# Kernel tuning notes

Measured on AMD Instinct MI355X. Metric: run time of the kernel, lower is better.

Reference implementation:

```python
import jax, jax.numpy as jnp
import numpy as np

B = 64        # graphs per batch
H = 8         # heads
EH = 16       # each_head = ceil(128/8)
HD = 128      # h_dimension
N_DA = 100000
N_Q = 20000
E_DA = 1000000
E_Q = 200000
EPS = 1e-5    # BatchNorm1d eps
SLOPE = 2.0   # leaky_relu_GAT_rate


def setup_inputs() -> dict:
    key = jax.random.key(0)
    ks = jax.random.split(key, 24)
    r = lambda i, shape, s=1.0: jax.random.normal(ks[i], shape, dtype=jnp.float32) * s
    return {
        'h_da_last': r(0, (N_DA, HD)),
        'h_q_last': r(1, (N_Q, HD)),
        'h_da_0': r(2, (N_DA, HD)),
        'h_q_0': r(3, (N_Q, HD)),
        'W_L': r(4, (HD, HD), 0.05), 'b_L': jnp.zeros((HD,), jnp.float32),
        'gateq_W': r(5, (HD, 1), 0.05), 'gateq_b': jnp.zeros((1,), jnp.float32),
        'gate1_W': r(6, (HD, 1), 0.05), 'gate1_b': jnp.zeros((1,), jnp.float32),
        'gate2_W': r(7, (HD, 1), 0.05), 'gate2_b': jnp.zeros((1,), jnp.float32),
        'Q_comb': r(8, (1, HD), 0.1),
        'Qf_W1': r(9, (HD, 2 * HD), 0.05), 'Qf_b1': jnp.zeros((2 * HD,), jnp.float32),
        'Qf_W2': r(10, (2 * HD, 2 * H * EH), 0.05), 'Qf_b2': jnp.zeros((2 * H * EH,), jnp.float32),
        'end_W1': r(11, (H * EH, 2 * HD), 0.05), 'end_b1': jnp.zeros((2 * HD,), jnp.float32),
        'end_W2': r(12, (2 * HD, HD), 0.05), 'end_b2': jnp.zeros((HD,), jnp.float32),
        'src_da': jax.random.randint(ks[13], (E_DA,), 0, N_DA),
        'dst_da': jax.random.randint(ks[14], (E_DA,), 0, N_DA),
        'src_q': jax.random.randint(ks[15], (E_Q,), 0, N_Q),
        'dst_q': jax.random.randint(ks[16], (E_Q,), 0, N_Q),
        'gid_da': jnp.sort(jax.random.randint(ks[17], (N_DA,), 0, B)),
        'gid_q': jnp.sort(jax.random.randint(ks[18], (N_Q,), 0, B)),
        'PEid': jax.random.randint(ks[19], (100000,), 0, E_DA),
        'DEid': jax.random.randint(ks[20], (100000,), 0, E_DA),
        'len_Mn': 5,
    }


def _bn(y):
    # BatchNorm1d(affine=False), training mode: biased batch stats
    mu = jnp.mean(y, axis=0)
    var = jnp.mean((y - mu) ** 2, axis=0)
    return (y - mu) / jnp.sqrt(var + EPS)


def _fnn(x, W1, b1, W2, b2):
    y = jax.nn.elu(_bn(x @ W1 + b1))
    return jax.nn.elu(_bn(y @ W2 + b2))


def _gap(W, b, feat, gid):
    # GlobalAttentionPooling: softmax(gate) over nodes per graph, weighted sum
    g = (feat @ W + b)[:, 0]                               # [N]
    m = jax.ops.segment_max(g, gid, num_segments=B)
    e = jnp.exp(g - m[gid])
    s = jax.ops.segment_sum(e, gid, num_segments=B)
    w = e / s[gid]
    return jax.ops.segment_sum(w[:, None] * feat, gid, num_segments=B)  # [B, HD]


def _edge_softmax(e, dst, n):
    # softmax over incoming edges per destination node, per head. e: [E, H, 1]
    m = jax.ops.segment_max(e, dst, num_segments=n)
    ex = jnp.exp(e - m[dst])
    s = jax.ops.segment_sum(ex, dst, num_segments=n)
    return ex / s[dst]


def forward(h_da_last, h_q_last, h_da_0, h_q_0, W_L, b_L, gateq_W, gateq_b,
            gate1_W, gate1_b, gate2_W, gate2_b, Q_comb, Qf_W1, Qf_b1, Qf_W2, Qf_b2,
            end_W1, end_b1, end_W2, end_b2,
            src_da, dst_da, src_q, dst_q, gid_da, gid_q, PEid, DEid, len_Mn):
    tmp_q = h_q_last  # MM is None branch

    # graph-level query representation -> per-graph attention queries Q [B, H, 2*EH]
    glq = _gap(gateq_W, gateq_b, h_q_last, gid_q)
    Q = _fnn(glq, Qf_W1, Qf_b1, Qf_W2, Qf_b2).reshape(B, H, 2 * EH)

    def att_comb(M1, M2, gid):
        # ATTpolling_for_3Dtensor with shared Q_comb
        k1 = _gap(gate1_W, gate1_b, M1, gid)
        k2 = _gap(gate2_W, gate2_b, M2, gid)
        s = jnp.stack([(Q_comb * k1).sum(-1), (Q_comb * k2).sum(-1)], axis=-1)  # [B, 2]
        a = jax.nn.softmax(s, axis=-1)[gid]                                     # [N, 2]
        return M1 * a[:, 0:1] + M2 * a[:, 1:2]

    def branch(h_last, tmp, h0, M2, src, dst, gid, n):
        Qn = Q[gid]                                  # [n, H, 2*EH]
        Ql, Qr = Qn[..., :EH], Qn[..., EH:]
        feat = (tmp @ W_L + b_L).reshape(n, H, EH)
        el = (feat * Ql).sum(-1, keepdims=True)      # [n, H, 1]
        er = (feat * Qr).sum(-1, keepdims=True)
        fh = att_comb(h0, M2, gid)
        ft = (fh @ W_L + b_L).reshape(n, H, EH)
        e = jax.nn.leaky_relu(el[src] + er[dst], negative_slope=SLOPE)  # [E, H, 1]
        a = _edge_softmax(e, dst, n)
        agg = jax.ops.segment_sum(ft[src] * a, dst, num_segments=n)     # [n, H, EH]
        out = _fnn(agg.reshape(n, H * EH), end_W1, end_b1, end_W2, end_b2)
        return h_last + out, a                       # residual=True

    h_q_next, _ = branch(h_q_last, tmp_q, h_q_0, h_q_last + (h_q_last - tmp_q),
                         src_q, dst_q, gid_q, N_Q)
    h_da_next, a_da = branch(h_da_last, h_da_last, h_da_0, h_da_last,
                             src_da, dst_da, gid_da, N_DA)

    PE = a_da[PEid].sum(axis=0)                      # [H, 1]
    DE = a_da[DEid].sum(axis=0)
    loss = -1.0 * jnp.mean((PE - DE) / len_Mn, axis=0).reshape(1, 1)
    return h_da_next, h_q_next, loss


def reference(h_da_last, h_q_last, h_da_0, h_q_0, W_L, b_L, gateq_W, gateq_b,
              gate1_W, gate1_b, gate2_W, gate2_b, Q_comb, Qf_W1, Qf_b1, Qf_W2, Qf_b2,
              end_W1, end_b1, end_W2, end_b2,
              src_da, dst_da, src_q, dst_q, gid_da, gid_q, PEid, DEid, len_Mn):
    return forward(h_da_last, h_q_last, h_da_0, h_q_0, W_L, b_L, gateq_W, gateq_b,
                   gate1_W, gate1_b, gate2_W, gate2_b, Q_comb, Qf_W1, Qf_b1, Qf_W2, Qf_b2,
                   end_W1, end_b1, end_W2, end_b2,
                   src_da, dst_da, src_q, dst_q, gid_da, gid_q, PEid, DEid, len_Mn)
```

## Files before the change

kernel.cpp:

```cpp
#include <hip/hip_runtime.h>
#include <math.h>

static constexpr int CB   = 64;
static constexpr int CH   = 8;
static constexpr int CEH  = 16;
static constexpr int CHD  = 128;
static constexpr int CNDA = 100000;
static constexpr int CNQ  = 20000;
static constexpr int CEDA = 1000000;
static constexpr int CEQ  = 200000;
static constexpr float CEPS = 1e-5f;
static constexpr float CSLOPE = 2.0f;

typedef unsigned short ushortt;
typedef __attribute__((ext_vector_type(8))) short bf16x8;
typedef __attribute__((ext_vector_type(4))) float f32x4;

__device__ __forceinline__ float ldf(const float* p) { return *p; }
__device__ __forceinline__ float ldf(const ushortt* p) {
  return __uint_as_float(((unsigned)*p) << 16);
}
__device__ __forceinline__ void stf(float* p, float v) { *p = v; }
__device__ __forceinline__ void stf(ushortt* p, float v) {
  unsigned u = __float_as_uint(v);
  u += 0x7fff + ((u >> 16) & 1);
  *p = (ushortt)(u >> 16);
}
__device__ __forceinline__ short f2bf(float v) {
  unsigned u = __float_as_uint(v);
  u += 0x7fff + ((u >> 16) & 1);
  return (short)(u >> 16);
}
__device__ __forceinline__ float bf2f(short b) {
  return __uint_as_float(((unsigned)(ushortt)b) << 16);
}

__global__ void k_zero(float* __restrict__ p, long n) {
  long i = (long)blockIdx.x * blockDim.x + threadIdx.x;
  long stride = (long)gridDim.x * blockDim.x;
  for (; i < n; i += stride) p[i] = 0.f;
}
static inline void zero_launch(void* p, long n, hipStream_t s) {
  long b = (n + 255) / 256;
  int blocks = (int)(b > 4096 ? 4096 : (b < 1 ? 1 : b));
  hipLaunchKernelGGL(k_zero, dim3(blocks), dim3(256), 0, s, (float*)p, n);
}

__global__ void k_binit(int* start, int n) {
  int i = threadIdx.x;
  if (i <= CB) start[i] = n;
}
__global__ void k_bmark(const int* __restrict__ gid, int n, int* __restrict__ start) {
  int i = blockIdx.x * blockDim.x + threadIdx.x;
  if (i >= n) return;
  int g = gid[i];
  if (i == 0 || gid[i - 1] != g) atomicMin(&start[g], i);
}
__global__ void k_bfix(int* start) {
  if (threadIdx.x == 0) {
    for (int g = CB - 1; g >= 0; --g)
      if (start[g] > start[g + 1]) start[g] = start[g + 1];
  }
}

__global__ void k_gate_dot(const float* __restrict__ feat, const float* __restrict__ gw,
                           const float* __restrict__ gb, float* __restrict__ g, int n) {
  int wave = (blockIdx.x * blockDim.x + threadIdx.x) >> 6;
  int lane = threadIdx.x & 63;
  if (wave >= n) return;
  const float* row = feat + (size_t)wave * CHD;
  float v = row[lane] * gw[lane] + row[lane + 64] * gw[lane + 64];
  for (int off = 32; off > 0; off >>= 1) v += __shfl_down(v, off, 64);
  if (lane == 0) g[wave] = v + gb[0];
}

__global__ void k_gate_dot2(const float* __restrict__ feat,
                            const float* __restrict__ w1, const float* __restrict__ b1,
                            const float* __restrict__ w2, const float* __restrict__ b2,
                            float* __restrict__ g1, float* __restrict__ g2, int n) {
  int wave = (blockIdx.x * blockDim.x + threadIdx.x) >> 6;
  int lane = threadIdx.x & 63;
  if (wave >= n) return;
  const float* row = feat + (size_t)wave * CHD;
  float r0 = row[lane], r1 = row[lane + 64];
  float v1 = r0 * w1[lane] + r1 * w1[lane + 64];
  float v2 = r0 * w2[lane] + r1 * w2[lane + 64];
  for (int off = 32; off > 0; off >>= 1) {
    v1 += __shfl_down(v1, off, 64);
    v2 += __shfl_down(v2, off, 64);
  }
  if (lane == 0) {
    g1[wave] = v1 + b1[0];
    g2[wave] = v2 + b2[0];
  }
}

__global__ void k_gmax5(const float* __restrict__ gq, const int* __restrict__ startq,
                        const int* __restrict__ startda, float* __restrict__ m) {
  int job = blockIdx.x >> 6, grp = blockIdx.x & 63;
  const float* g;
  const int* start;
  if (job == 0)      { g = gq;                              start = startq; }
  else if (job == 1) { g = gq + 2 * (size_t)CNQ;            start = startq; }
  else if (job == 2) { g = gq + (size_t)CNQ;                start = startq; }
  else if (job == 3) { g = gq + 3 * (size_t)CNQ;            start = startda; }
  else               { g = gq + 3 * (size_t)CNQ + CNDA;     start = startda; }
  int s0 = start[grp], s1 = start[grp + 1];
  int t = threadIdx.x;
  __shared__ float red[256];
  float v = -1e30f;
  for (int i = s0 + t; i < s1; i += 256) v = fmaxf(v, g[i]);
  red[t] = v;
  __syncthreads();
  for (int o = 128; o > 0; o >>= 1) {
    if (t < o) red[t] = fmaxf(red[t], red[t + o]);
    __syncthreads();
  }
  if (t == 0) m[job * 64 + grp] = red[0];
}

template <int NG>
__global__ __launch_bounds__(128) void k_gap_partial(
    const float* __restrict__ g0, const float* __restrict__ g1,
    const float* __restrict__ feat, const int* __restrict__ start,
    const float* __restrict__ m,
    float* __restrict__ acc0, float* __restrict__ acc1,
    float* __restrict__ sums) {
  int grp = blockIdx.x;
  int s0 = start[grp], s1 = start[grp + 1];
  int len = s1 - s0;
  if (len <= 0) return;
  int NC = gridDim.y;
  int per = (len + NC - 1) / NC;
  int r0 = s0 + blockIdx.y * per;
  int r1 = min(s1, r0 + per);
  if (r0 >= r1) return;
  int t = threadIdx.x;
  float m0 = m[grp];
  float m1 = (NG == 2) ? m[64 + grp] : 0.f;
  float a0 = 0.f, a1 = 0.f, sum0 = 0.f, sum1 = 0.f;
  for (int i = r0; i < r1; ++i) {
    float f = feat[(size_t)i * CHD + t];
    float e0 = expf(g0[i] - m0);
    sum0 += e0;
    a0 += e0 * f;
    if (NG == 2) {
      float e1 = expf(g1[i] - m1);
      sum1 += e1;
      a1 += e1 * f;
    }
  }
  atomicAdd(&acc0[grp * CHD + t], a0);
  if (NG == 2) atomicAdd(&acc1[grp * CHD + t], a1);
  if (t == 0) {
    atomicAdd(&sums[grp], sum0);
    if (NG == 2) atomicAdd(&sums[64 + grp], sum1);
  }
}

__global__ void k_gap_norm5(float* __restrict__ glq, const float* __restrict__ sbuf) {
  int job = blockIdx.x >> 6, grp = blockIdx.x & 63;
  int t = threadIdx.x;
  int smap = (job == 1) ? 2 : ((job == 2) ? 1 : job);
  float sv = sbuf[smap * 64 + grp];
  float* acc = glq + (size_t)job * CB * CHD + grp * CHD;
  float v = acc[t];
  acc[t] = (sv > 0.f) ? v / sv : 0.f;
}

__global__ void k_mm_small(const float* __restrict__ X, const float* __restrict__ W,
                           const float* __restrict__ bias, float* __restrict__ Y,
                           int m, int k, int p) {
  int idx = blockIdx.x * blockDim.x + threadIdx.x;
  if (idx >= m * p) return;
  int r = idx / p, c = idx % p;
  const float* xr = X + (size_t)r * k;
  const float* wc = W + c;
  float acc = bias[c];
  int kk = 0;
  for (; kk + 8 <= k; kk += 8) {
    float xv[8], wv[8];
#pragma unroll
    for (int j = 0; j < 8; ++j) {
      xv[j] = xr[kk + j];
      wv[j] = wc[(size_t)(kk + j) * p];
    }
#pragma unroll
    for (int j = 0; j < 8; ++j) acc += xv[j] * wv[j];
  }
  for (; kk < k; ++kk) acc += xr[kk] * wc[(size_t)kk * p];
  Y[idx] = acc;
}

__global__ void k_bn_elu_small(float* __restrict__ Y, int m, int p) {
  int c = blockIdx.x * blockDim.x + threadIdx.x;
  if (c >= p) return;
  float s = 0.f, s2 = 0.f;
  int i = 0;
  for (; i + 8 <= m; i += 8) {
    float v[8];
#pragma unroll
    for (int j = 0; j < 8; ++j) v[j] = Y[(size_t)(i + j) * p + c];
#pragma unroll
    for (int j = 0; j < 8; ++j) { s += v[j]; s2 += v[j] * v[j]; }
  }
  for (; i < m; ++i) {
    float v = Y[(size_t)i * p + c];
    s += v; s2 += v * v;
  }
  float mu = s / m;
  float var = s2 / m - mu * mu;
  float inv = rsqrtf(var + CEPS);
  i = 0;
  for (; i + 8 <= m; i += 8) {
    float v[8];
#pragma unroll
    for (int j = 0; j < 8; ++j) v[j] = Y[(size_t)(i + j) * p + c];
#pragma unroll
    for (int j = 0; j < 8; ++j) {
      float x = (v[j] - mu) * inv;
      Y[(size_t)(i + j) * p + c] = x > 0.f ? x : expm1f(x);
    }
  }
  for (; i < m; ++i) {
    float x = (Y[(size_t)i * p + c] - mu) * inv;
    Y[(size_t)i * p + c] = x > 0.f ? x : expm1f(x);
  }
}

__global__ void k_attcomb(const float* __restrict__ k1, const float* __restrict__ k2,
                          const float* __restrict__ Qc, float* __restrict__ a) {
  int grp = blockIdx.x;
  int t = threadIdx.x;
  float v1 = Qc[t] * k1[grp * CHD + t] + Qc[t + 64] * k1[grp * CHD + t + 64];
  float v2 = Qc[t] * k2[grp * CHD + t] + Qc[t + 64] * k2[grp * CHD + t + 64];
  for (int off = 32; off > 0; off >>= 1) {
    v1 += __shfl_down(v1, off, 64);
    v2 += __shfl_down(v2, off, 64);
  }
  if (t == 0) {
    float mx = fmaxf(v1, v2);
    float e1 = expf(v1 - mx), e2 = expf(v2 - mx);
    float s = e1 + e2;
    a[grp * 2] = e1 / s;
    a[grp * 2 + 1] = e2 / s;
  }
}

__global__ void k_wq(const float* __restrict__ W_L, const float* __restrict__ b_L,
                     const float* __restrict__ Qm, float* __restrict__ WQ,
                     float* __restrict__ bQ) {
  int g = blockIdx.x;
  int t = threadIdx.x;
  for (int j = 0; j < 8; ++j) {
    int idx = t + j * 256;
    int d = idx >> 4, c = idx & 15;
    int h = c & 7, off = (c >= 8) ? CEH : 0;
    const float* w = W_L + d * CHD + h * CEH;
    const float* q = Qm + g * 256 + h * 32 + off;
    float acc = 0.f;
#pragma unroll
    for (int e = 0; e < CEH; ++e) acc += w[e] * q[e];
    WQ[g * 2048 + idx] = acc;
  }
  if (t < 16) {
    int c = t, h = c & 7, off = (c >= 8) ? CEH : 0;
    const float* b = b_L + h * CEH;
    const float* q = Qm + g * 256 + h * 32 + off;
    float acc = 0.f;
#pragma unroll
    for (int e = 0; e < CEH; ++e) acc += b[e] * q[e];
    bQ[g * 16 + c] = acc;
  }
}

__global__ void k_eler(const float* __restrict__ tmp, const float* __restrict__ WQ,
                       const float* __restrict__ bQ, const int* __restrict__ gid,
                       float* __restrict__ elr, int n) {
  int idx = blockIdx.x * blockDim.x + threadIdx.x;
  if (idx >= n * 16) return;
  int i = idx >> 4, c = idx & 15;
  int g = gid[i];
  const float* wq = WQ + g * 2048 + c;
  const float* row = tmp + (size_t)i * CHD;
  float acc = bQ[g * 16 + c];
#pragma unroll 4
  for (int d = 0; d < CHD; ++d) acc += row[d] * wq[d * 16];
  elr[idx] = acc;
}

__global__ void k_tcast(const float* __restrict__ W, ushortt* __restrict__ WT,
                        int K, int P) {
  int i = blockIdx.x * blockDim.x + threadIdx.x;
  if (i >= K * P) return;
  int p = i / K, k = i % K;
  stf(&WT[i], W[(size_t)k * P + p]);
}

template <int P>
__global__ void k_bn_prep(const float* __restrict__ stats, float* __restrict__ pr, int n) {
  int c = threadIdx.x;
  if (c >= P) return;
  float invn = 1.f / (float)n;
  float mu = stats[c] * invn;
  float var = stats[P + c] * invn - mu * mu;
  pr[c] = mu;
  pr[P + c] = rsqrtf(var + CEPS);
}

template <int TP>
__global__ void k_stats_reduce(const float* __restrict__ pstat, float* __restrict__ stats,
                               int nb) {
  int c = blockIdx.x * blockDim.x + threadIdx.x;
  if (c >= TP) return;
  int NC = gridDim.y;
  int per = (nb + NC - 1) / NC;
  int r0 = blockIdx.y * per;
  int r1 = min(nb, r0 + per);
  if (r0 >= r1) return;
  float s0 = 0.f, s1 = 0.f, s2 = 0.f, s3 = 0.f;
  int r = r0;
  for (; r + 4 <= r1; r += 4) {
    s0 += pstat[(size_t)(r + 0) * TP + c];
    s1 += pstat[(size_t)(r + 1) * TP + c];
    s2 += pstat[(size_t)(r + 2) * TP + c];
    s3 += pstat[(size_t)(r + 3) * TP + c];
  }
  for (; r < r1; ++r) s0 += pstat[(size_t)r * TP + c];
  atomicAdd(&stats[c], (s0 + s1) + (s2 + s3));
}

template <int K, int P, int XM, bool STATS, typename OT>
__global__ __launch_bounds__(256, 2) void k_gemm_mfma(
    const void* __restrict__ X0v, const void* __restrict__ X1v,
    const float* __restrict__ acomb, const int* __restrict__ gid,
    const float* __restrict__ bnmu, const float* __restrict__ bninv,
    const ushortt* __restrict__ BT, const float* __restrict__ bias,
    OT* __restrict__ Y, float* __restrict__ pstat, int n) {
  constexpr int NT = P / 16;
  const int wave = threadIdx.x >> 6, lane = threadIdx.x & 63;
  const int quad = lane >> 4, l16 = lane & 15;
  const int r0w = blockIdx.x * 64 + wave * 16;
  const int rA = r0w + l16;
  const bool rowok = rA < n;
  f32x4 acc[NT];
#pragma unroll
  for (int t = 0; t < NT; ++t) acc[t] = f32x4{0.f, 0.f, 0.f, 0.f};
  float a0 = 0.f, a1 = 0.f;
  if (XM == 1 && rowok) {
    int g = gid[rA];
    a0 = acomb[2 * g];
    a1 = acomb[2 * g + 1];
  }
  for (int k0 = 0; k0 < K; k0 += 32) {
    const int kk = k0 + quad * 8;
    bf16x8 af = {};
    if (rowok) {
      if constexpr (XM == 2) {
        af = *(const bf16x8*)((const ushortt*)X0v + (size_t)rA * K + kk);
      } else if constexpr (XM == 3) {
        bf16x8 raw = *(const bf16x8*)((const ushortt*)X0v + (size_t)rA * K + kk);
#pragma unroll
        for (int j = 0; j < 8; ++j) {
          float v = bf2f(raw[j]);
          v = (v - bnmu[kk + j]) * bninv[kk + j];
          v = v > 0.f ? v : (__expf(v) - 1.f);
          af[j] = f2bf(v);
        }
      } else {
        const float* px = (const float*)X0v + (size_t)rA * K + kk;
        float v[8];
        if constexpr (XM == 1) {
          const float* py = (const float*)X1v + (size_t)rA * K + kk;
#pragma unroll
          for (int j = 0; j < 8; ++j) v[j] = a0 * px[j] + a1 * py[j];
        } else {
#pragma unroll
          for (int j = 0; j < 8; ++j) v[j] = px[j];
        }
#pragma unroll
        for (int j = 0; j < 8; ++j) af[j] = f2bf(v[j]);
      }
    }
    bf16x8 bfr[NT];
#pragma unroll
    for (int t = 0; t < NT; ++t)
      bfr[t] = *(const bf16x8*)(BT + (size_t)(t * 16 + l16) * K + kk);
#pragma unroll
    for (int t = 0; t < NT; ++t)
      acc[t] = __builtin_amdgcn_mfma_f32_16x16x32_bf16(af, bfr[t], acc[t], 0, 0, 0);
  }
  float* pw = STATS ? (pstat + ((size_t)blockIdx.x * 4 + wave) * (2 * P)) : nullptr;
#pragma unroll
  for (int t = 0; t < NT; ++t) {
    const int c = t * 16 + l16;
    float b = bias[c];
    float s = 0.f, s2 = 0.f;
#pragma unroll
    for (int r = 0; r < 4; ++r) {
      int gr = r0w + quad * 4 + r;
      if (gr < n) {
        float val = acc[t][r] + b;
        stf(Y + (size_t)gr * P + c, val);
        if constexpr (STATS) {
          float vq = (sizeof(OT) == 2) ? bf2f(f2bf(val)) : val;
          s += vq;
          s2 += vq * vq;
        }
      }
    }
    if constexpr (STATS) {
      s += __shfl_xor(s, 16, 64);
      s += __shfl_xor(s, 32, 64);
      s2 += __shfl_xor(s2, 16, 64);
      s2 += __shfl_xor(s2, 32, 64);
      if (quad == 0) {
        pw[c] = s;
        pw[P + c] = s2;
      }
    }
  }
}

__global__ void k_count(const int* __restrict__ dst, int* __restrict__ counts, int E) {
  int e = blockIdx.x * blockDim.x + threadIdx.x;
  if (e < E) atomicAdd(&counts[dst[e]], 1);
}
__global__ void k_scan_reduce(const int* __restrict__ counts, int* __restrict__ bsum, int n) {
  __shared__ int red[256];
  int t = threadIdx.x;
  int base = blockIdx.x * 1024;
  int s = 0;
  for (int j = 0; j < 4; ++j) {
    int i = base + t * 4 + j;
    if (i < n) s += counts[i];
  }
  red[t] = s;
  __syncthreads();
  for (int o = 128; o > 0; o >>= 1) {
    if (t < o) red[t] += red[t + o];
    __syncthreads();
  }
  if (t == 0) bsum[blockIdx.x] = red[0];
}
__global__ void k_scan_top(int* __restrict__ bsum, int nb) {
  __shared__ int sh[128];
  int t = threadIdx.x;
  int v = (t < nb) ? bsum[t] : 0;
  sh[t] = v;
  __syncthreads();
  for (int o = 1; o < 128; o <<= 1) {
    int x = (t >= o) ? sh[t - o] : 0;
    __syncthreads();
    sh[t] += x;
    __syncthreads();
  }
  if (t < nb) bsum[t] = sh[t] - v;
}
__global__ void k_scan_final(const int* __restrict__ counts, const int* __restrict__ bsum,
                             int* __restrict__ rowptr, int n, int E) {
  __shared__ int sh[256];
  int t = threadIdx.x;
  int base = blockIdx.x * 1024;
  int v[4];
  int s = 0;
  for (int j = 0; j < 4; ++j) {
    int i = base + t * 4 + j;
    v[j] = (i < n) ? counts[i] : 0;
    s += v[j];
  }
  sh[t] = s;
  __syncthreads();
  for (int o = 1; o < 256; o <<= 1) {
    int x = (t >= o) ? sh[t - o] : 0;
    __syncthreads();
    sh[t] += x;
    __syncthreads();
  }
  int off = bsum[blockIdx.x] + sh[t] - s;
  for (int j = 0; j < 4; ++j) {
    int i = base + t * 4 + j;
    if (i < n) rowptr[i] = off;
    off += v[j];
  }
  if (blockIdx.x == 0 && t == 0) rowptr[n] = E;
}
__global__ void k_copy_int(const int* __restrict__ a, int* __restrict__ b, int n) {
  int i = blockIdx.x * blockDim.x + threadIdx.x;
  if (i < n) b[i] = a[i];
}
__global__ void k_scatter(const int* __restrict__ dst, const int* __restrict__ srcA,
                          int* __restrict__ cursor, int* __restrict__ csr_src, int E) {
  int e = blockIdx.x * blockDim.x + threadIdx.x;
  if (e >= E) return;
  int d = dst[e];
  int pos = atomicAdd(&cursor[d], 1);
  csr_src[pos] = srcA[e];
}

__global__ __launch_bounds__(256) void k_node_agg(
    const int* __restrict__ rowptr, const int* __restrict__ csr_src,
    const float* __restrict__ elr, const ushortt* __restrict__ ft,
    float* __restrict__ agg, float* __restrict__ mOut, float* __restrict__ sOut, int n) {
  int node = blockIdx.x * 4 + (threadIdx.x >> 6);
  if (node >= n) return;
  int lane = threadIdx.x & 63;
  int h_p = lane & 7;
  int e_loc = lane >> 3;
  int h_a = lane >> 3;
  int s0 = rowptr[node], s1 = rowptr[node + 1];
  if (s1 <= s0) {
    *(float2*)(agg + (size_t)node * CHD + lane * 2) = make_float2(0.f, 0.f);
    if (lane < 8) {
      mOut[(size_t)node * CH + lane] = -1e30f;
      sOut[(size_t)node * CH + lane] = 0.f;
    }
    return;
  }
  float erd_p = elr[(size_t)node * 16 + 8 + h_p];
  float mx = -1e30f;
  for (int base = s0; base < s1; base += 8) {
    int e = base + e_loc;
    if (e < s1) {
      int sj = csr_src[e];
      mx = fmaxf(mx, elr[(size_t)sj * 16 + h_p]);
    }
  }
  mx = fmaxf(mx, __shfl_xor(mx, 8, 64));
  mx = fmaxf(mx, __shfl_xor(mx, 16, 64));
  mx = fmaxf(mx, __shfl_xor(mx, 32, 64));
  float xm = mx + erd_p;
  float m_p = xm >= 0.f ? xm : CSLOPE * xm;
  float s_part = 0.f, a0 = 0.f, a1 = 0.f;
  int base = s0;
  for (; base + 8 <= s1; base += 8) {
    int sj = csr_src[base + e_loc];
    float x = elr[(size_t)sj * 16 + h_p] + erd_p;
    x = x >= 0.f ? x : CSLOPE * x;
    float p = __expf(x - m_p);
    s_part += p;
#pragma unroll
    for (int e = 0; e < 8; ++e) {
      float pe = __shfl(p, e * 8 + h_a, 64);
      int se = __shfl(sj, e * 8, 64);
      unsigned ftv = *(const unsigned*)(ft + (size_t)se * CHD + lane * 2);
      a0 += pe * __uint_as_float(ftv << 16);
      a1 += pe * __uint_as_float(ftv & 0xffff0000u);
    }
  }
  if (base < s1) {
    int cnt = s1 - base;
    int sj = 0;
    float p = 0.f;
    if (e_loc < cnt) {
      sj = csr_src[base + e_loc];
      float x = elr[(size_t)sj * 16 + h_p] + erd_p;
      x = x >= 0.f ? x : CSLOPE * x;
      p = __expf(x - m_p);
      s_part += p;
    }
    for (int e = 0; e < cnt; ++e) {
      float pe = __shfl(p, e * 8 + h_a, 64);
      int se = __shfl(sj, e * 8, 64);
      unsigned ftv = *(const unsigned*)(ft + (size_t)se * CHD + lane * 2);
      a0 += pe * __uint_as_float(ftv << 16);
      a1 += pe * __uint_as_float(ftv & 0xffff0000u);
    }
  }
  s_part += __shfl_xor(s_part, 8, 64);
  s_part += __shfl_xor(s_part, 16, 64);
  s_part += __shfl_xor(s_part, 32, 64);
  float s_acc = __shfl(s_part, h_a, 64);
  float inv = 1.f / s_acc;
  float2 o;
  o.x = a0 * inv;
  o.y = a1 * inv;
  *(float2*)(agg + (size_t)node * CHD + lane * 2) = o;
  if (lane < 8) {
    mOut[(size_t)node * CH + lane] = m_p;
    sOut[(size_t)node * CH + lane] = s_part;
  }
}

template <int P, bool RESID, typename T>
__global__ void k_bn_apply(T* __restrict__ Y, const float* __restrict__ stats,
                           const float* __restrict__ hlast, int n) {
  size_t idx = (size_t)blockIdx.x * blockDim.x + threadIdx.x;
  if (idx >= (size_t)n * P) return;
  int c = (int)(idx % P);
  float invn = 1.f / (float)n;
  float mu = stats[c] * invn;
  float var = stats[P + c] * invn - mu * mu;
  float v = (ldf(Y + idx) - mu) * rsqrtf(var + CEPS);
  v = v > 0.f ? v : expm1f(v);
  if (RESID) v += hlast[idx];
  stf(Y + idx, v);
}

__device__ __forceinline__ float attn_val(int e, int h, const int* __restrict__ src,
                                          const int* __restrict__ dst,
                                          const float* __restrict__ elr,
                                          const float* __restrict__ mOut,
                                          const float* __restrict__ sOut) {
  int ss = src[e], sd = dst[e];
  float x = elr[(size_t)ss * 16 + h] + elr[(size_t)sd * 16 + 8 + h];
  x = x >= 0.f ? x : CSLOPE * x;
  return expf(x - mOut[(size_t)sd * CH + h]) / sOut[(size_t)sd * CH + h];
}

__global__ void k_pd(const int* __restrict__ src, const int* __restrict__ dst,
                     const float* __restrict__ elr, const float* __restrict__ mOut,
                     const float* __restrict__ sOut, const int* __restrict__ PEid,
                     const int* __restrict__ DEid, float* __restrict__ pdp,
                     int nPE, int nDE) {
  __shared__ float part[CH];
  if (threadIdx.x < CH) part[threadIdx.x] = 0.f;
  __syncthreads();
  int idx = blockIdx.x * blockDim.x + threadIdx.x;
  int j = idx >> 3, h = idx & 7;
  float acc = 0.f;
  if (j < nPE) acc += attn_val(PEid[j], h, src, dst, elr, mOut, sOut);
  if (j < nDE) acc -= attn_val(DEid[j], h, src, dst, elr, mOut, sOut);
  atomicAdd(&part[h], acc);
  __syncthreads();
  if (threadIdx.x < CH) pdp[(size_t)blockIdx.x * CH + threadIdx.x] = part[threadIdx.x];
}
__global__ void k_loss(const float* __restrict__ pdp, int nb,
                       const int* __restrict__ lenMn, float* __restrict__ out) {
  __shared__ float part[CH];
  int t = threadIdx.x;
  if (t < CH) part[t] = 0.f;
  __syncthreads();
  int h = t & 7;
  float acc = 0.f;
  for (int j = t >> 3; j < nb; j += 32) acc += pdp[(size_t)j * CH + h];
  atomicAdd(&part[h], acc);
  __syncthreads();
  if (t == 0) {
    float len = (float)lenMn[0];
    float s = 0.f;
    for (int hh = 0; hh < CH; ++hh) s += part[hh] / len;
    out[0] = -s / (float)CH;
  }
}

static void run_branch(int n, int E, const float* h_last, const float* h0,
                       const int* src, const int* dst, const int* gid,
                       const float* acomb, const float* WQ, const float* bQ,
                       const ushortt* W_LT, const float* b_L,
                       const ushortt* W1T, const float* end_b1,
                       const ushortt* W2T, const float* end_b2,
                       float* U, float* elr, float* mOut, float* sOut,
                       int* counts, int* rowptr, int* cursor, int* csr_src, int* bsum,
                       float* stats ,
                       float* bnpr , float* pstat, float* out, hipStream_t stream) {
  ushortt* ftB = (ushortt*)U;
  ushortt* y1B = (ushortt*)U;
  float* stats1 = stats;
  float* stats2 = stats + 512;
  int nChunks = (n + 1023) / 1024;
  int nbG = (n + 63) / 64;
  int nbW = nbG * 4;
  zero_launch(counts, n, stream);
  zero_launch(stats, 1024, stream);
  hipLaunchKernelGGL(k_count, dim3((E + 255) / 256), dim3(256), 0, stream, dst, counts, E);
  hipLaunchKernelGGL(k_scan_reduce, dim3(nChunks), dim3(256), 0, stream, counts, bsum, n);
  hipLaunchKernelGGL(k_scan_top, dim3(1), dim3(128), 0, stream, bsum, nChunks);
  hipLaunchKernelGGL(k_scan_final, dim3(nChunks), dim3(256), 0, stream, counts, bsum, rowptr, n, E);
  hipLaunchKernelGGL(k_copy_int, dim3((n + 255) / 256), dim3(256), 0, stream, rowptr, cursor, n);
  hipLaunchKernelGGL(k_scatter, dim3((E + 255) / 256), dim3(256), 0, stream, dst, src, cursor, csr_src, E);
  hipLaunchKernelGGL(k_eler, dim3((n * 16 + 255) / 256), dim3(256), 0, stream,
                     h_last, WQ, bQ, gid, elr, n);
  hipLaunchKernelGGL((k_gemm_mfma<128, 128, 1, false, ushortt>), dim3(nbG),
                     dim3(256), 0, stream, h0, h_last, acomb, gid,
                     (const float*)nullptr, (const float*)nullptr,
                     W_LT, b_L, ftB, (float*)nullptr, n);
  hipLaunchKernelGGL(k_node_agg, dim3((n + 3) / 4), dim3(256), 0, stream,
                     rowptr, csr_src, elr, ftB, out, mOut, sOut, n);
  hipLaunchKernelGGL((k_gemm_mfma<128, 256, 0, true, ushortt>), dim3(nbG),
                     dim3(256), 0, stream, out, (const void*)nullptr,
                     (const float*)nullptr, (const int*)nullptr,
                     (const float*)nullptr, (const float*)nullptr,
                     W1T, end_b1, y1B, pstat, n);
  hipLaunchKernelGGL((k_stats_reduce<512>), dim3(2, 64), dim3(256), 0, stream,
                     pstat, stats1, nbW);
  hipLaunchKernelGGL((k_bn_prep<256>), dim3(1), dim3(256), 0, stream, stats1, bnpr, n);
  hipLaunchKernelGGL((k_gemm_mfma<256, 128, 3, true, float>), dim3(nbG),
                     dim3(256), 0, stream, y1B, (const void*)nullptr,
                     (const float*)nullptr, (const int*)nullptr,
                     bnpr, bnpr + 256,
                     W2T, end_b2, out, pstat, n);
  hipLaunchKernelGGL((k_stats_reduce<256>), dim3(1, 64), dim3(256), 0, stream,
                     pstat, stats2, nbW);
  hipLaunchKernelGGL((k_bn_apply<128, true, float>),
                     dim3((int)(((size_t)n * 128 + 255) / 256)), dim3(256), 0, stream,
                     out, stats2, h_last, n);
}

extern "C" void kernel_launch(void* const* d_in, const int* in_sizes, int n_in,
                              void* d_out, int out_size, void* d_ws, size_t ws_size,
                              hipStream_t stream) {
  const float* h_da_last = (const float*)d_in[0];
  const float* h_q_last  = (const float*)d_in[1];
  const float* h_da_0    = (const float*)d_in[2];
  const float* h_q_0     = (const float*)d_in[3];
  const float* W_L       = (const float*)d_in[4];
  const float* b_L       = (const float*)d_in[5];
  const float* gateq_W   = (const float*)d_in[6];
  const float* gateq_b   = (const float*)d_in[7];
  const float* gate1_W   = (const float*)d_in[8];
  const float* gate1_b   = (const float*)d_in[9];
  const float* gate2_W   = (const float*)d_in[10];
  const float* gate2_b   = (const float*)d_in[11];
  const float* Q_comb    = (const float*)d_in[12];
  const float* Qf_W1     = (const float*)d_in[13];
  const float* Qf_b1     = (const float*)d_in[14];
  const float* Qf_W2     = (const float*)d_in[15];
  const float* Qf_b2     = (const float*)d_in[16];
  const float* end_W1    = (const float*)d_in[17];
  const float* end_b1    = (const float*)d_in[18];
  const float* end_W2    = (const float*)d_in[19];
  const float* end_b2    = (const float*)d_in[20];
  const int* src_da = (const int*)d_in[21];
  const int* dst_da = (const int*)d_in[22];
  const int* src_q  = (const int*)d_in[23];
  const int* dst_q  = (const int*)d_in[24];
  const int* gid_da = (const int*)d_in[25];
  const int* gid_q  = (const int*)d_in[26];
  const int* PEid   = (const int*)d_in[27];
  const int* DEid   = (const int*)d_in[28];
  const int* len_Mn = (const int*)d_in[29];

  float* out_da   = (float*)d_out;
  float* out_q    = (float*)d_out + (size_t)CNDA * CHD;
  float* out_loss = (float*)d_out + (size_t)CNDA * CHD + (size_t)CNQ * CHD;

  float* ws = (float*)d_ws;
  size_t off = 0;
  auto alloc = [&](size_t cnt) { float* p = ws + off; off += cnt; return p; };
  float* U    = alloc((size_t)CNDA * 128);
  float* elr  = alloc((size_t)CNDA * 16);
  float* mOut = alloc((size_t)CNDA * CH);
  float* sOut = alloc((size_t)CNDA * CH);
  int* counts  = (int*)alloc(CNDA);
  int* rowptr  = (int*)alloc(CNDA + 4);
  int* cursor  = (int*)alloc(CNDA);
  int* csr_src = (int*)alloc(CEDA);
  int* bsum    = (int*)alloc(128);
  ushortt* W_LT = (ushortt*)alloc(128 * 128 / 2);
  ushortt* W1T  = (ushortt*)alloc(128 * 256 / 2);
  ushortt* W2T  = (ushortt*)alloc(256 * 128 / 2);
  float* WQ   = alloc((size_t)CB * 2048);
  float* bQ   = alloc((size_t)CB * 16);
  float* gq   = alloc(CNQ);
  float* g1q  = alloc(CNQ);
  float* g2q  = alloc(CNQ);
  float* g1da = alloc(CNDA);
  float* g2da = alloc(CNDA);
  float* glq  = alloc(CB * CHD);
  float* k1q  = alloc(CB * CHD);
  float* k2q  = alloc(CB * CHD);
  float* k1da = alloc(CB * CHD);
  float* k2da = alloc(CB * CHD);
  float* Qt   = alloc(CB * 256);
  float* Qm   = alloc(CB * 256);
  float* acq  = alloc(CB * 2);
  float* acda = alloc(CB * 2);
  float* stats = alloc(1024);
  float* bnpr  = alloc(512);
  float* mbuf  = alloc(5 * 64);
  float* sbuf  = alloc(5 * 64);
  int* startq  = (int*)alloc(68);
  int* startda = (int*)alloc(68);
  float* pstat = alloc(((size_t)(CNDA + 63) / 64) * 4 * 512);
  float* pdp   = alloc(((size_t)CNDA * CH + 255) / 256 * CH);
  (void)ws_size; (void)n_in; (void)out_size;

  hipLaunchKernelGGL(k_tcast, dim3((128 * 128 + 255) / 256), dim3(256), 0, stream, W_L, W_LT, 128, 128);
  hipLaunchKernelGGL(k_tcast, dim3((128 * 256 + 255) / 256), dim3(256), 0, stream, end_W1, W1T, 128, 256);
  hipLaunchKernelGGL(k_tcast, dim3((256 * 128 + 255) / 256), dim3(256), 0, stream, end_W2, W2T, 256, 128);

  hipLaunchKernelGGL(k_binit, dim3(1), dim3(128), 0, stream, startq, CNQ);
  hipLaunchKernelGGL(k_binit, dim3(1), dim3(128), 0, stream, startda, CNDA);
  hipLaunchKernelGGL(k_bmark, dim3((CNQ + 255) / 256), dim3(256), 0, stream, gid_q, CNQ, startq);
  hipLaunchKernelGGL(k_bmark, dim3((CNDA + 255) / 256), dim3(256), 0, stream, gid_da, CNDA, startda);
  hipLaunchKernelGGL(k_bfix, dim3(1), dim3(64), 0, stream, startq);
  hipLaunchKernelGGL(k_bfix, dim3(1), dim3(64), 0, stream, startda);

  hipLaunchKernelGGL(k_gate_dot2, dim3((CNQ + 3) / 4), dim3(256), 0, stream,
                     h_q_last, gateq_W, gateq_b, gate2_W, gate2_b, gq, g2q, CNQ);
  hipLaunchKernelGGL(k_gate_dot, dim3((CNQ + 3) / 4), dim3(256), 0, stream, h_q_0, gate1_W, gate1_b, g1q, CNQ);
  hipLaunchKernelGGL(k_gate_dot, dim3((CNDA + 3) / 4), dim3(256), 0, stream, h_da_0, gate1_W, gate1_b, g1da, CNDA);
  hipLaunchKernelGGL(k_gate_dot, dim3((CNDA + 3) / 4), dim3(256), 0, stream, h_da_last, gate2_W, gate2_b, g2da, CNDA);

  hipLaunchKernelGGL(k_gmax5, dim3(5 * CB), dim3(256), 0, stream, gq, startq, startda, mbuf);
  zero_launch(glq, 5 * (size_t)CB * CHD, stream);
  zero_launch(sbuf, 5 * 64, stream);
  hipLaunchKernelGGL((k_gap_partial<2>), dim3(CB, 32), dim3(128), 0, stream,
                     gq, g2q, h_q_last, startq, mbuf + 0, glq, k2q, sbuf + 0);
  hipLaunchKernelGGL((k_gap_partial<1>), dim3(CB, 32), dim3(128), 0, stream,
                     g1q, (const float*)nullptr, h_q_0, startq, mbuf + 128,
                     k1q, (float*)nullptr, sbuf + 128);
  hipLaunchKernelGGL((k_gap_partial<1>), dim3(CB, 32), dim3(128), 0, stream,
                     g1da, (const float*)nullptr, h_da_0, startda, mbuf + 192,
                     k1da, (float*)nullptr, sbuf + 192);
  hipLaunchKernelGGL((k_gap_partial<1>), dim3(CB, 32), dim3(128), 0, stream,
                     g2da, (const float*)nullptr, h_da_last, startda, mbuf + 256,
                     k2da, (float*)nullptr, sbuf + 256);
  hipLaunchKernelGGL(k_gap_norm5, dim3(5 * CB), dim3(128), 0, stream, glq, sbuf);

  hipLaunchKernelGGL(k_mm_small, dim3((CB * 256 + 255) / 256), dim3(256), 0, stream,
                     glq, Qf_W1, Qf_b1, Qt, CB, 128, 256);
  hipLaunchKernelGGL(k_bn_elu_small, dim3(1), dim3(256), 0, stream, Qt, CB, 256);
  hipLaunchKernelGGL(k_mm_small, dim3((CB * 256 + 255) / 256), dim3(256), 0, stream,
                     Qt, Qf_W2, Qf_b2, Qm, CB, 256, 256);
  hipLaunchKernelGGL(k_bn_elu_small, dim3(1), dim3(256), 0, stream, Qm, CB, 256);

  hipLaunchKernelGGL(k_wq, dim3(CB), dim3(256), 0, stream, W_L, b_L, Qm, WQ, bQ);

  hipLaunchKernelGGL(k_attcomb, dim3(CB), dim3(64), 0, stream, k1q, k2q, Q_comb, acq);
  hipLaunchKernelGGL(k_attcomb, dim3(CB), dim3(64), 0, stream, k1da, k2da, Q_comb, acda);

  run_branch(CNQ, CEQ, h_q_last, h_q_0, src_q, dst_q, gid_q, acq, WQ, bQ,
             W_LT, b_L, W1T, end_b1, W2T, end_b2,
             U, elr, mOut, sOut, counts, rowptr, cursor, csr_src, bsum,
             stats, bnpr, pstat, out_q, stream);

  run_branch(CNDA, CEDA, h_da_last, h_da_0, src_da, dst_da, gid_da, acda, WQ, bQ,
             W_LT, b_L, W1T, end_b1, W2T, end_b2,
             U, elr, mOut, sOut, counts, rowptr, cursor, csr_src, bsum,
             stats, bnpr, pstat, out_da, stream);

  int nPE = in_sizes[27], nDE = in_sizes[28];
  int nMax = nPE > nDE ? nPE : nDE;
  int nbPD = (nMax * CH + 255) / 256;
  hipLaunchKernelGGL(k_pd, dim3(nbPD), dim3(256), 0, stream,
                     src_da, dst_da, elr, mOut, sOut, PEid, DEid, pdp, nPE, nDE);
  hipLaunchKernelGGL(k_loss, dim3(1), dim3(256), 0, stream, pdp, nbPD, len_Mn, out_loss);
}
```

Measured before the change: 1.143 ms.

## Use global per-head max as softmax shift, vectorize BN apply, fast exp

Adds a small kernel that computes a global per-head maximum of the source attention logits, using an order-preserving unsigned encoding and atomicMax. The node aggregation kernel now builds its softmax shift from that maximum instead of doing its own gather pass over each node's edges. This removes one full edge traversal, and the tail loop is merged into a fully unrolled loop. The trade-off is a risk of underflow when a node's logits sit far below the global maximum. The change also vectorizes the final BatchNorm-ELU-residual kernel with float4 and swaps expf for __expf in several places, giving up a little accuracy.

```diff
diff --git a/kernel.cpp b/kernel.cpp
--- a/kernel.cpp
+++ b/kernel.cpp
@@ -33,6 +33,14 @@
 }
 __device__ __forceinline__ float bf2f(short b) {
   return __uint_as_float(((unsigned)(ushortt)b) << 16);
+}
+__device__ __forceinline__ unsigned fenc(float f) {
+  unsigned b = __float_as_uint(f);
+  return (b & 0x80000000u) ? ~b : (b | 0x80000000u);
+}
+__device__ __forceinline__ float fdec(unsigned u) {
+  unsigned b = (u & 0x80000000u) ? (u ^ 0x80000000u) : ~u;
+  return __uint_as_float(b);
 }
 
 __global__ void k_zero(float* __restrict__ p, long n) {
@@ -141,11 +149,11 @@
   float a0 = 0.f, a1 = 0.f, sum0 = 0.f, sum1 = 0.f;
   for (int i = r0; i < r1; ++i) {
     float f = feat[(size_t)i * CHD + t];
-    float e0 = expf(g0[i] - m0);
+    float e0 = __expf(g0[i] - m0);
     sum0 += e0;
     a0 += e0 * f;
     if (NG == 2) {
-      float e1 = expf(g1[i] - m1);
+      float e1 = __expf(g1[i] - m1);
       sum1 += e1;
       a1 += e1 * f;
     }
@@ -287,6 +295,24 @@
 #pragma unroll 4
   for (int d = 0; d < CHD; ++d) acc += row[d] * wq[d * 16];
   elr[idx] = acc;
+}
+
+__global__ void k_elmax(const float* __restrict__ elr, unsigned* __restrict__ mgl, int n) {
+  int h = blockIdx.x;
+  int chunk = blockIdx.y;
+  int per = (n + 31) / 32;
+  int i0 = chunk * per, i1 = min(n, i0 + per);
+  int t = threadIdx.x;
+  __shared__ float red[256];
+  float v = -1e30f;
+  for (int i = i0 + t; i < i1; i += 256) v = fmaxf(v, elr[(size_t)i * 16 + h]);
+  red[t] = v;
+  __syncthreads();
+  for (int o = 128; o > 0; o >>= 1) {
+    if (t < o) red[t] = fmaxf(red[t], red[t + o]);
+    __syncthreads();
+  }
+  if (t == 0) atomicMax(&mgl[h], fenc(red[0]));
 }
 
 __global__ void k_tcast(const float* __restrict__ W, ushortt* __restrict__ WT,
@@ -500,7 +526,8 @@
 
 __global__ __launch_bounds__(256) void k_node_agg(
     const int* __restrict__ rowptr, const int* __restrict__ csr_src,
-    const float* __restrict__ elr, const ushortt* __restrict__ ft,
+    const float* __restrict__ elr, const unsigned* __restrict__ mgl,
+    const ushortt* __restrict__ ft,
     float* __restrict__ agg, float* __restrict__ mOut, float* __restrict__ sOut, int n) {
   int node = blockIdx.x * 4 + (threadIdx.x >> 6);
   if (node >= n) return;
@@ -518,37 +545,10 @@
     return;
   }
   float erd_p = elr[(size_t)node * 16 + 8 + h_p];
-  float mx = -1e30f;
-  for (int base = s0; base < s1; base += 8) {
-    int e = base + e_loc;
-    if (e < s1) {
-      int sj = csr_src[e];
-      mx = fmaxf(mx, elr[(size_t)sj * 16 + h_p]);
-    }
-  }
-  mx = fmaxf(mx, __shfl_xor(mx, 8, 64));
-  mx = fmaxf(mx, __shfl_xor(mx, 16, 64));
-  mx = fmaxf(mx, __shfl_xor(mx, 32, 64));
-  float xm = mx + erd_p;
+  float xm = fdec(mgl[h_p]) + erd_p;
   float m_p = xm >= 0.f ? xm : CSLOPE * xm;
   float s_part = 0.f, a0 = 0.f, a1 = 0.f;
-  int base = s0;
-  for (; base + 8 <= s1; base += 8) {
-    int sj = csr_src[base + e_loc];
-    float x = elr[(size_t)sj * 16 + h_p] + erd_p;
-    x = x >= 0.f ? x : CSLOPE * x;
-    float p = __expf(x - m_p);
-    s_part += p;
-#pragma unroll
-    for (int e = 0; e < 8; ++e) {
-      float pe = __shfl(p, e * 8 + h_a, 64);
-      int se = __shfl(sj, e * 8, 64);
-      unsigned ftv = *(const unsigned*)(ft + (size_t)se * CHD + lane * 2);
-      a0 += pe * __uint_as_float(ftv << 16);
-      a1 += pe * __uint_as_float(ftv & 0xffff0000u);
-    }
-  }
-  if (base < s1) {
+  for (int base = s0; base < s1; base += 8) {
     int cnt = s1 - base;
     int sj = 0;
     float p = 0.f;
@@ -559,7 +559,8 @@
       p = __expf(x - m_p);
       s_part += p;
     }
-    for (int e = 0; e < cnt; ++e) {
+#pragma unroll
+    for (int e = 0; e < 8; ++e) {
       float pe = __shfl(p, e * 8 + h_a, 64);
       int se = __shfl(sj, e * 8, 64);
       unsigned ftv = *(const unsigned*)(ft + (size_t)se * CHD + lane * 2);
@@ -582,19 +583,26 @@
   }
 }
 
-template <int P, bool RESID, typename T>
-__global__ void k_bn_apply(T* __restrict__ Y, const float* __restrict__ stats,
-                           const float* __restrict__ hlast, int n) {
-  size_t idx = (size_t)blockIdx.x * blockDim.x + threadIdx.x;
-  if (idx >= (size_t)n * P) return;
-  int c = (int)(idx % P);
+__global__ void k_bn_apply_f4(float* __restrict__ Y, const float* __restrict__ stats,
+                              const float* __restrict__ hlast, int n) {
+  int idx = blockIdx.x * blockDim.x + threadIdx.x;
+  if (idx >= n * 32) return;
+  int cg = (idx & 31) * 4;
   float invn = 1.f / (float)n;
-  float mu = stats[c] * invn;
-  float var = stats[P + c] * invn - mu * mu;
-  float v = (ldf(Y + idx) - mu) * rsqrtf(var + CEPS);
-  v = v > 0.f ? v : expm1f(v);
-  if (RESID) v += hlast[idx];
-  stf(Y + idx, v);
+  float4 y = ((const float4*)Y)[idx];
+  float4 hl = ((const float4*)hlast)[idx];
+  float yy[4] = {y.x, y.y, y.z, y.w};
+  float hh[4] = {hl.x, hl.y, hl.z, hl.w};
+  float o[4];
+#pragma unroll
+  for (int j = 0; j < 4; ++j) {
+    float mu = stats[cg + j] * invn;
+    float var = stats[128 + cg + j] * invn - mu * mu;
+    float v = (yy[j] - mu) * rsqrtf(var + CEPS);
+    v = v > 0.f ? v : (__expf(v) - 1.f);
+    o[j] = v + hh[j];
+  }
+  ((float4*)Y)[idx] = make_float4(o[0], o[1], o[2], o[3]);
 }
 
 __device__ __forceinline__ float attn_val(int e, int h, const int* __restrict__ src,
@@ -605,7 +613,7 @@
   int ss = src[e], sd = dst[e];
   float x = elr[(size_t)ss * 16 + h] + elr[(size_t)sd * 16 + 8 + h];
   x = x >= 0.f ? x : CSLOPE * x;
-  return expf(x - mOut[(size_t)sd * CH + h]) / sOut[(size_t)sd * CH + h];
+  return __expf(x - mOut[(size_t)sd * CH + h]) / sOut[(size_t)sd * CH + h];
 }
 
 __global__ void k_pd(const int* __restrict__ src, const int* __restrict__ dst,
@@ -650,7 +658,7 @@
                        const ushortt* W_LT, const float* b_L,
                        const ushortt* W1T, const float* end_b1,
                        const ushortt* W2T, const float* end_b2,
-                       float* U, float* elr, float* mOut, float* sOut,
+                       float* U, float* elr, unsigned* mgl, float* mOut, float* sOut,
                        int* counts, int* rowptr, int* cursor, int* csr_src, int* bsum,
                        float* stats ,
                        float* bnpr , float* pstat, float* out, hipStream_t stream) {
@@ -663,6 +671,7 @@
   int nbW = nbG * 4;
   zero_launch(counts, n, stream);
   zero_launch(stats, 1024, stream);
+  zero_launch(mgl, 8, stream);
   hipLaunchKernelGGL(k_count, dim3((E + 255) / 256), dim3(256), 0, stream, dst, counts, E);
   hipLaunchKernelGGL(k_scan_reduce, dim3(nChunks), dim3(256), 0, stream, counts, bsum, n);
   hipLaunchKernelGGL(k_scan_top, dim3(1), dim3(128), 0, stream, bsum, nChunks);
@@ -671,12 +680,13 @@
   hipLaunchKernelGGL(k_scatter, dim3((E + 255) / 256), dim3(256), 0, stream, dst, src, cursor, csr_src, E);
   hipLaunchKernelGGL(k_eler, dim3((n * 16 + 255) / 256), dim3(256), 0, stream,
                      h_last, WQ, bQ, gid, elr, n);
+  hipLaunchKernelGGL(k_elmax, dim3(8, 32), dim3(256), 0, stream, elr, mgl, n);
   hipLaunchKernelGGL((k_gemm_mfma<128, 128, 1, false, ushortt>), dim3(nbG),
                      dim3(256), 0, stream, h0, h_last, acomb, gid,
                      (const float*)nullptr, (const float*)nullptr,
                      W_LT, b_L, ftB, (float*)nullptr, n);
   hipLaunchKernelGGL(k_node_agg, dim3((n + 3) / 4), dim3(256), 0, stream,
-                     rowptr, csr_src, elr, ftB, out, mOut, sOut, n);
+                     rowptr, csr_src, elr, mgl, ftB, out, mOut, sOut, n);
   hipLaunchKernelGGL((k_gemm_mfma<128, 256, 0, true, ushortt>), dim3(nbG),
                      dim3(256), 0, stream, out, (const void*)nullptr,
                      (const float*)nullptr, (const int*)nullptr,
@@ -692,8 +702,7 @@
                      W2T, end_b2, out, pstat, n);
   hipLaunchKernelGGL((k_stats_reduce<256>), dim3(1, 64), dim3(256), 0, stream,
                      pstat, stats2, nbW);
-  hipLaunchKernelGGL((k_bn_apply<128, true, float>),
-                     dim3((int)(((size_t)n * 128 + 255) / 256)), dim3(256), 0, stream,
+  hipLaunchKernelGGL(k_bn_apply_f4, dim3((n * 32 + 255) / 256), dim3(256), 0, stream,
                      out, stats2, h_last, n);
 }
 
@@ -768,6 +777,7 @@
   float* acda = alloc(CB * 2);
   float* stats = alloc(1024);
   float* bnpr  = alloc(512);
+  unsigned* mgl = (unsigned*)alloc(8);
   float* mbuf  = alloc(5 * 64);
   float* sbuf  = alloc(5 * 64);
   int* startq  = (int*)alloc(68);
@@ -823,12 +833,12 @@
 
   run_branch(CNQ, CEQ, h_q_last, h_q_0, src_q, dst_q, gid_q, acq, WQ, bQ,
              W_LT, b_L, W1T, end_b1, W2T, end_b2,
-             U, elr, mOut, sOut, counts, rowptr, cursor, csr_src, bsum,
+             U, elr, mgl, mOut, sOut, counts, rowptr, cursor, csr_src, bsum,
              stats, bnpr, pstat, out_q, stream);
 
   run_branch(CNDA, CEDA, h_da_last, h_da_0, src_da, dst_da, gid_da, acda, WQ, bQ,
              W_LT, b_L, W1T, end_b1, W2T, end_b2,
-             U, elr, mOut, sOut, counts, rowptr, cursor, csr_src, bsum,
+             U, elr, mgl, mOut, sOut, counts, rowptr, cursor, csr_src, bsum,
              stats, bnpr, pstat, out_da, stream);
 
   int nPE = in_sizes[27], nDE = in_sizes[28];
```

Measured after the change: 1.102 ms. 3.6% less time.
